# Kernel tuning notes

Hardware: AMD Instinct MI355X
Metric: run time of the kernel (lower is better)

## Reference

```python
import jax, jax.numpy as jnp
import numpy as np

MEM, KD, VD, H, TEMP = 4096, 512, 512, 8, 1.0
B, N, BW = 4, 1024, 1024


def setup_inputs() -> dict:
    key = jax.random.key(0)
    ks = jax.random.split(key, 9)
    s = 0.02
    return {
        "queries": jax.random.normal(ks[0], (B, N, KD), jnp.float32),
        "write_keys": jax.random.normal(ks[1], (BW, KD), jnp.float32),
        "write_values": jax.random.normal(ks[2], (BW, VD), jnp.float32),
        "mem_keys": jax.random.normal(ks[3], (MEM, KD), jnp.float32),
        "mem_values": jax.random.normal(ks[4], (MEM, VD), jnp.float32),
        "Wq": jax.random.normal(ks[5], (KD, KD * H), jnp.float32) * s,
        "bq": jnp.zeros((KD * H,), jnp.float32),
        "Wvp": jax.random.normal(ks[6], (H * VD, VD), jnp.float32) * s,
        "bvp": jnp.zeros((VD,), jnp.float32),
        "Wg": jax.random.normal(ks[7], (KD + VD, KD), jnp.float32) * s,
        "bg": jnp.zeros((KD,), jnp.float32),
    }


def _read(queries, mem_keys, mem_values, Wq, bq, Wvp, bvp):
    b, n, _ = queries.shape
    q = queries @ Wq + bq                       # [b, n, H*KD]
    q = q.reshape(b, n, H, KD).transpose(0, 2, 1, 3)  # [b, h, n, d]
    # keys/values are shared across batch & heads: contract directly, no repeat
    scores = jnp.einsum('bhnd,md->bhnm', q, mem_keys) / (KD ** 0.5) / TEMP
    attn = jax.nn.softmax(scores, axis=-1)
    rv = jnp.einsum('bhnm,md->bhnd', attn, mem_values)  # [b, h, n, VD]
    rv = rv.transpose(0, 2, 1, 3).reshape(b, n, H * VD)
    return rv @ Wvp + bvp                        # [b, n, VD]


def _write(write_keys, write_values, mem_keys, mem_values, Wg, bg):
    eps = 1e-8
    kn = write_keys / jnp.maximum(jnp.linalg.norm(write_keys, axis=-1, keepdims=True), eps)
    mn = mem_keys / jnp.maximum(jnp.linalg.norm(mem_keys, axis=-1, keepdims=True), eps)
    idx = jnp.argmax(kn @ mn.T, axis=1)          # [BW] fixed against original keys

    def step(carry, inp):
        K, V = carry
        k, v, i = inp
        combined = jnp.concatenate([k, V[i]], axis=-1)   # reads current values
        gate = jax.nn.sigmoid(combined @ Wg + bg)        # [KD]
        K = K.at[i].set(gate * k + (1.0 - gate) * K[i])
        V = V.at[i].set(gate * v + (1.0 - gate) * V[i])
        return (K, V), None

    (nk, nv), _ = jax.lax.scan(step, (mem_keys, mem_values), (write_keys, write_values, idx))
    return nk, nv


def reference(queries, write_keys, write_values, mem_keys, mem_values, Wq, bq, Wvp, bvp, Wg, bg):
    read_out = _read(queries, mem_keys, mem_values, Wq, bq, Wvp, bvp)
    new_keys, new_values = _write(write_keys, write_values, mem_keys, mem_values, Wg, bg)
    return read_out, new_keys, new_values
```

## Files before the change

kernel.cpp:

```cpp
#include <hip/hip_runtime.h>
#include <cstdint>
#include <cstddef>

typedef __attribute__((ext_vector_type(8))) short short8;
typedef __attribute__((ext_vector_type(4))) float f32x4;
typedef __attribute__((ext_vector_type(4))) int i32x4;
typedef __attribute__((ext_vector_type(8))) int i32x8;
typedef unsigned char u8;
typedef unsigned short u16;
typedef unsigned int u32;
typedef unsigned long long u64;

__device__ __forceinline__ u16 f2bf(float f) {
    u32 u = __float_as_uint(f);
    u = (u + 0x7FFFu + ((u >> 16) & 1u)) >> 16;
    return (u16)u;
}
__device__ __forceinline__ float bf2f(u16 h) {
    u32 u = ((u32)h) << 16;
    return __uint_as_float(u);
}
__device__ __forceinline__ u8 f2fp8(float f) {
    return (u8)(__builtin_amdgcn_cvt_pk_fp8_f32(f, f, 0, false) & 0xFF);
}

__device__ __forceinline__ void gl_lds16(const void* g, void* l) {
    __builtin_amdgcn_global_load_lds((const __attribute__((address_space(1))) void*)g,
                                     (__attribute__((address_space(3))) void*)l, 16, 0, 0);
}

__global__ void cast_bf16_kernel(const float* __restrict__ src, u16* __restrict__ dst) {
    int i = blockIdx.x * 256 + threadIdx.x;
    float4 v = *((const float4*)src + i);
    ushort4 r;
    r.x = f2bf(v.x); r.y = f2bf(v.y); r.z = f2bf(v.z); r.w = f2bf(v.w);
    *((ushort4*)dst + i) = r;
}

__global__ void split_bf16_kernel(const float* __restrict__ src,
                                  u16* __restrict__ hi, u16* __restrict__ lo) {
    int i = blockIdx.x * 256 + threadIdx.x;
    float4 v = *((const float4*)src + i);
    ushort4 h, l;
    h.x = f2bf(v.x); l.x = f2bf(v.x - bf2f(h.x));
    h.y = f2bf(v.y); l.y = f2bf(v.y - bf2f(h.y));
    h.z = f2bf(v.z); l.z = f2bf(v.z - bf2f(h.z));
    h.w = f2bf(v.w); l.w = f2bf(v.w - bf2f(h.w));
    *((ushort4*)hi + i) = h;
    *((ushort4*)lo + i) = l;
}

__global__ void cast_transpose_kernel(const float* __restrict__ src, u16* __restrict__ dst,
                                      int R, int C) {
    __shared__ float tile[32][33];
    int tx = threadIdx.x & 31, ty = threadIdx.x >> 5;
    int c0 = blockIdx.x * 32, r0 = blockIdx.y * 32;
#pragma unroll
    for (int j = 0; j < 4; j++)
        tile[ty + 8 * j][tx] = src[(size_t)(r0 + ty + 8 * j) * C + c0 + tx];
    __syncthreads();
#pragma unroll
    for (int j = 0; j < 4; j++)
        dst[(size_t)(c0 + ty + 8 * j) * R + r0 + tx] = f2bf(tile[tx][ty + 8 * j]);
}

__global__ void cast_transpose_fp8_kernel(const float* __restrict__ src, u8* __restrict__ dst,
                                          int R, int C) {
    __shared__ float tile[32][33];
    int tx = threadIdx.x & 31, ty = threadIdx.x >> 5;
    int c0 = blockIdx.x * 32, r0 = blockIdx.y * 32;
#pragma unroll
    for (int j = 0; j < 4; j++)
        tile[ty + 8 * j][tx] = src[(size_t)(r0 + ty + 8 * j) * C + c0 + tx];
    __syncthreads();
#pragma unroll
    for (int j = 0; j < 4; j++)
        dst[(size_t)(c0 + ty + 8 * j) * R + r0 + tx] = f2fp8(tile[tx][ty + 8 * j]);
}

__global__ __launch_bounds__(256) void key_prep_kernel(const float* __restrict__ mk,
                                                       u16* __restrict__ mn_hi,
                                                       u16* __restrict__ mn_lo,
                                                       u16* __restrict__ Kb) {
    int row = blockIdx.x, tid = threadIdx.x;
    const float* src = mk + (size_t)row * 512;
    float x0 = src[tid], x1 = src[tid + 256];
    float ss = x0 * x0 + x1 * x1;
#pragma unroll
    for (int m = 1; m < 64; m <<= 1) ss += __shfl_xor(ss, m);
    __shared__ float sred[4];
    if ((tid & 63) == 0) sred[tid >> 6] = ss;
    __syncthreads();
    float tot = sred[0] + sred[1] + sred[2] + sred[3];
    float inv = 1.0f / fmaxf(sqrtf(tot), 1e-8f);
    float n0 = x0 * inv, n1 = x1 * inv;
    u16 h0 = f2bf(n0), h1 = f2bf(n1);
    mn_hi[(size_t)row * 512 + tid] = h0;
    mn_hi[(size_t)row * 512 + tid + 256] = h1;
    mn_lo[(size_t)row * 512 + tid] = f2bf(n0 - bf2f(h0));
    mn_lo[(size_t)row * 512 + tid + 256] = f2bf(n1 - bf2f(h1));
    Kb[(size_t)row * 512 + tid] = f2bf(x0);
    Kb[(size_t)row * 512 + tid + 256] = f2bf(x1);
}

template <int BN, int EPI>
__global__ __launch_bounds__(256, 2) void gemm_bt_kernel(const u16* __restrict__ A,
                                                         const u16* __restrict__ Bt,
                                                         const float* __restrict__ bias,
                                                         void* __restrict__ Cout,
                                                         int M, int N, int K) {
    constexpr int NT = BN / 32;
    __shared__ __align__(16) u16 A_lds[128 * 32];
    __shared__ __align__(16) u16 B_lds[BN * 32];
    int tid = threadIdx.x;
    int w = tid >> 6, lane = tid & 63, l15 = lane & 15, quad = lane >> 4;
    int wm = w >> 1, wn = w & 1;
    int n0 = blockIdx.x * BN, m0 = blockIdx.y * 128;
    int sa = (l15 >> 1) & 3;

    f32x4 acc[4][NT];
#pragma unroll
    for (int i = 0; i < 4; i++)
#pragma unroll
        for (int j = 0; j < NT; j++) acc[i][j] = (f32x4)(0.0f);

    for (int kt = 0; kt < K; kt += 32) {
        __syncthreads();
#pragma unroll
        for (int i = 0; i < 2; i++) {
            int c = i * 256 + tid;
            int r = c >> 2, s = (c & 3) ^ ((r >> 1) & 3);
            gl_lds16(&A[(size_t)(m0 + r) * K + kt + s * 8], &A_lds[c * 8]);
        }
#pragma unroll
        for (int i = 0; i < BN / 64; i++) {
            int c = i * 256 + tid;
            int r = c >> 2, s = (c & 3) ^ ((r >> 1) & 3);
            gl_lds16(&Bt[(size_t)(n0 + r) * K + kt + s * 8], &B_lds[c * 8]);
        }
        __syncthreads();
        short8 af[4], bf[NT];
#pragma unroll
        for (int mt = 0; mt < 4; mt++)
            af[mt] = *(const short8*)&A_lds[(wm * 64 + mt * 16 + l15) * 32 + (quad ^ sa) * 8];
#pragma unroll
        for (int nt = 0; nt < NT; nt++)
            bf[nt] = *(const short8*)&B_lds[(wn * (BN / 2) + nt * 16 + l15) * 32 + (quad ^ sa) * 8];
#pragma unroll
        for (int mt = 0; mt < 4; mt++)
#pragma unroll
            for (int nt = 0; nt < NT; nt++)
                acc[mt][nt] = __builtin_amdgcn_mfma_f32_16x16x32_bf16(af[mt], bf[nt], acc[mt][nt], 0, 0, 0);
    }

#pragma unroll
    for (int nt = 0; nt < NT; nt++) {
        int col = n0 + wn * (BN / 2) + nt * 16 + l15;
        float bs = bias[col];
#pragma unroll
        for (int mt = 0; mt < 4; mt++) {
            int row = m0 + wm * 64 + mt * 16 + quad * 4;
#pragma unroll
            for (int r = 0; r < 4; r++) {
                float v = acc[mt][nt][r] + bs;
                if (EPI == 0) {
                    ((float*)Cout)[(size_t)(row + r) * N + col] = v;
                } else {
                    int rr = row + r;
                    int bi = rr >> 10, ni = rr & 1023;
                    int h = col >> 9, d = col & 511;
                    ((u16*)Cout)[(((size_t)((bi * 8 + h)) * 1024 + ni)) * 512 + d] = f2bf(v);
                }
            }
        }
    }
}

__global__ __launch_bounds__(256, 2) void s_exp_gemm_kernel(const u16* __restrict__ Q,
                                                            const u16* __restrict__ Kb,
                                                            u8* __restrict__ P,
                                                            float* __restrict__ denom) {
    __shared__ __align__(16) u16 A_lds[128 * 32];
    __shared__ __align__(16) u16 B_lds[128 * 32];
    int tid = threadIdx.x;
    int w = tid >> 6, lane = tid & 63, l15 = lane & 15, quad = lane >> 4;
    int wm = w >> 1, wn = w & 1;
    int s0 = blockIdx.x * 128, q0 = blockIdx.y * 128;
    int sa = (l15 >> 1) & 3;

    f32x4 acc[4][4];
#pragma unroll
    for (int i = 0; i < 4; i++)
#pragma unroll
        for (int j = 0; j < 4; j++) acc[i][j] = (f32x4)(0.0f);

    for (int kt = 0; kt < 512; kt += 32) {
        __syncthreads();
#pragma unroll
        for (int i = 0; i < 2; i++) {
            int c = i * 256 + tid;
            int r = c >> 2, s = (c & 3) ^ ((r >> 1) & 3);
            gl_lds16(&Kb[(size_t)(s0 + r) * 512 + kt + s * 8], &A_lds[c * 8]);
            gl_lds16(&Q[(size_t)(q0 + r) * 512 + kt + s * 8], &B_lds[c * 8]);
        }
        __syncthreads();
        short8 af[4], bf[4];
#pragma unroll
        for (int mt = 0; mt < 4; mt++)
            af[mt] = *(const short8*)&A_lds[(wm * 64 + mt * 16 + l15) * 32 + (quad ^ sa) * 8];
#pragma unroll
        for (int nt = 0; nt < 4; nt++)
            bf[nt] = *(const short8*)&B_lds[(wn * 64 + nt * 16 + l15) * 32 + (quad ^ sa) * 8];
#pragma unroll
        for (int mt = 0; mt < 4; mt++)
#pragma unroll
            for (int nt = 0; nt < 4; nt++)
                acc[mt][nt] = __builtin_amdgcn_mfma_f32_16x16x32_bf16(af[mt], bf[nt], acc[mt][nt], 0, 0, 0);
    }

    const float sc = 0.06375871826463886f;
#pragma unroll
    for (int nt = 0; nt < 4; nt++) {
        int q = q0 + wn * 64 + nt * 16 + l15;
        float rs = 0.f;
#pragma unroll
        for (int mt = 0; mt < 4; mt++) {
            float p0 = exp2f(acc[mt][nt][0] * sc);
            float p1 = exp2f(acc[mt][nt][1] * sc);
            float p2 = exp2f(acc[mt][nt][2] * sc);
            float p3 = exp2f(acc[mt][nt][3] * sc);
            rs += (p0 + p1) + (p2 + p3);
            u32 lo = (u32)__builtin_amdgcn_cvt_pk_fp8_f32(p0, p1, 0, false);
            u32 dw = (u32)__builtin_amdgcn_cvt_pk_fp8_f32(p2, p3, (int)lo, true);
            int col = s0 + wm * 64 + mt * 16 + quad * 4;
            *(u32*)&P[(size_t)q * 4096 + col] = dw;
        }
        rs += __shfl_xor(rs, 16);
        rs += __shfl_xor(rs, 32);
        if (quad == 0) atomicAdd(&denom[q], rs);
    }
}

__global__ __launch_bounds__(256, 2) void pv_gemm_kernel(const u8* __restrict__ P,
                                                         const u8* __restrict__ Vt8,
                                                         const float* __restrict__ denom,
                                                         u16* __restrict__ rv,
                                                         int bh0) {
    __shared__ __align__(16) u8 A_lds[128 * 128];
    __shared__ __align__(16) u8 B_lds[128 * 128];
    int tid = threadIdx.x;
    int w = tid >> 6, lane = tid & 63, l15 = lane & 15, quad = lane >> 4;
    int wm = w >> 1, wn = w & 1;
    int d0 = blockIdx.x * 128, q0 = blockIdx.y * 128;

    f32x4 acc[4][4];
#pragma unroll
    for (int i = 0; i < 4; i++)
#pragma unroll
        for (int j = 0; j < 4; j++) acc[i][j] = (f32x4)(0.0f);

    for (int kt = 0; kt < 4096; kt += 128) {
        __syncthreads();
#pragma unroll
        for (int i = 0; i < 4; i++) {
            int c = i * 256 + tid;
            int r = c >> 3, s = (c & 7) ^ (r & 7);
            gl_lds16(&Vt8[(size_t)(d0 + r) * 4096 + kt + s * 16], &A_lds[c * 16]);
            gl_lds16(&P[(size_t)(q0 + r) * 4096 + kt + s * 16], &B_lds[c * 16]);
        }
        __syncthreads();
        i32x8 af[4], bf[4];
#pragma unroll
        for (int mt = 0; mt < 4; mt++) {
            int row = wm * 64 + mt * 16 + l15;
            const u8* pa = &A_lds[row * 128];
            int sl0 = (quad * 2) ^ (row & 7), sl1 = (quad * 2 + 1) ^ (row & 7);
            i32x4 lo = *(const i32x4*)&pa[sl0 * 16];
            i32x4 hi = *(const i32x4*)&pa[sl1 * 16];
            af[mt] = __builtin_shufflevector(lo, hi, 0, 1, 2, 3, 4, 5, 6, 7);
        }
#pragma unroll
        for (int nt = 0; nt < 4; nt++) {
            int row = wn * 64 + nt * 16 + l15;
            const u8* pb = &B_lds[row * 128];
            int sl0 = (quad * 2) ^ (row & 7), sl1 = (quad * 2 + 1) ^ (row & 7);
            i32x4 lo = *(const i32x4*)&pb[sl0 * 16];
            i32x4 hi = *(const i32x4*)&pb[sl1 * 16];
            bf[nt] = __builtin_shufflevector(lo, hi, 0, 1, 2, 3, 4, 5, 6, 7);
        }
#pragma unroll
        for (int mt = 0; mt < 4; mt++)
#pragma unroll
            for (int nt = 0; nt < 4; nt++)
                acc[mt][nt] = __builtin_amdgcn_mfma_scale_f32_16x16x128_f8f6f4(
                    af[mt], bf[nt], acc[mt][nt], 0, 0,
                    0, 0x7F7F7F7F, 0, 0x7F7F7F7F);
    }

#pragma unroll
    for (int nt = 0; nt < 4; nt++) {
        int lq = q0 + wn * 64 + nt * 16 + l15;
        int gr = bh0 * 1024 + lq;
        float inv = 1.0f / denom[lq];
        int b = gr >> 13, h = (gr >> 10) & 7, n = gr & 1023;
        size_t base = ((size_t)(b * 1024 + n)) * 4096 + h * 512;
#pragma unroll
        for (int mt = 0; mt < 4; mt++) {
            int d = d0 + wm * 64 + mt * 16 + quad * 4;
            ushort4 v4;
            v4.x = f2bf(acc[mt][nt][0] * inv);
            v4.y = f2bf(acc[mt][nt][1] * inv);
            v4.z = f2bf(acc[mt][nt][2] * inv);
            v4.w = f2bf(acc[mt][nt][3] * inv);
            *(ushort4*)&rv[base + d] = v4;
        }
    }
}

__global__ __launch_bounds__(256, 2) void sims_mfma_kernel(const u16* __restrict__ Ah,
                                                           const u16* __restrict__ Al,
                                                           const u16* __restrict__ Bh,
                                                           const u16* __restrict__ Bl,
                                                           u64* __restrict__ amax) {
    __shared__ __align__(16) u16 Ah_lds[128 * 32];
    __shared__ __align__(16) u16 Al_lds[128 * 32];
    __shared__ __align__(16) u16 Bh_lds[128 * 32];
    __shared__ __align__(16) u16 Bl_lds[128 * 32];
    int tid = threadIdx.x;
    int w = tid >> 6, lane = tid & 63, l15 = lane & 15, quad = lane >> 4;
    int wm = w >> 1, wn = w & 1;
    int n0 = blockIdx.x * 128, m0 = blockIdx.y * 128;
    int sa = (l15 >> 1) & 3;

    f32x4 acc[4][4];
#pragma unroll
    for (int i = 0; i < 4; i++)
#pragma unroll
        for (int j = 0; j < 4; j++) acc[i][j] = (f32x4)(0.0f);

    for (int kt = 0; kt < 512; kt += 32) {
        __syncthreads();
#pragma unroll
        for (int i = 0; i < 2; i++) {
            int c = i * 256 + tid;
            int r = c >> 2, s = (c & 3) ^ ((r >> 1) & 3);
            size_t ga = (size_t)(m0 + r) * 512 + kt + s * 8;
            size_t gb = (size_t)(n0 + r) * 512 + kt + s * 8;
            gl_lds16(&Ah[ga], &Ah_lds[c * 8]);
            gl_lds16(&Al[ga], &Al_lds[c * 8]);
            gl_lds16(&Bh[gb], &Bh_lds[c * 8]);
            gl_lds16(&Bl[gb], &Bl_lds[c * 8]);
        }
        __syncthreads();
        short8 afh[4], afl[4], bfh[4], bfl[4];
#pragma unroll
        for (int mt = 0; mt < 4; mt++) {
            int off = (wm * 64 + mt * 16 + l15) * 32 + (quad ^ sa) * 8;
            afh[mt] = *(const short8*)&Ah_lds[off];
            afl[mt] = *(const short8*)&Al_lds[off];
        }
#pragma unroll
        for (int nt = 0; nt < 4; nt++) {
            int off = (wn * 64 + nt * 16 + l15) * 32 + (quad ^ sa) * 8;
            bfh[nt] = *(const short8*)&Bh_lds[off];
            bfl[nt] = *(const short8*)&Bl_lds[off];
        }
#pragma unroll
        for (int mt = 0; mt < 4; mt++)
#pragma unroll
            for (int nt = 0; nt < 4; nt++) {
                acc[mt][nt] = __builtin_amdgcn_mfma_f32_16x16x32_bf16(afh[mt], bfh[nt], acc[mt][nt], 0, 0, 0);
                acc[mt][nt] = __builtin_amdgcn_mfma_f32_16x16x32_bf16(afh[mt], bfl[nt], acc[mt][nt], 0, 0, 0);
                acc[mt][nt] = __builtin_amdgcn_mfma_f32_16x16x32_bf16(afl[mt], bfh[nt], acc[mt][nt], 0, 0, 0);
            }
    }

#pragma unroll
    for (int mt = 0; mt < 4; mt++) {
#pragma unroll
        for (int r = 0; r < 4; r++) {
            int row = m0 + wm * 64 + mt * 16 + quad * 4 + r;
            u64 best = 0;
#pragma unroll
            for (int nt = 0; nt < 4; nt++) {
                int col = n0 + wn * 64 + nt * 16 + l15;
                u32 bb = __float_as_uint(acc[mt][nt][r]);
                bb = (bb & 0x80000000u) ? ~bb : (bb | 0x80000000u);
                u64 key = ((u64)bb << 32) | (u32)(4095 - col);
                best = best > key ? best : key;
            }
            u64 o;
            o = __shfl_xor(best, 1); best = best > o ? best : o;
            o = __shfl_xor(best, 2); best = best > o ? best : o;
            o = __shfl_xor(best, 4); best = best > o ? best : o;
            o = __shfl_xor(best, 8); best = best > o ? best : o;
            if (l15 == 0) atomicMax(&amax[row], best);
        }
    }
}

__global__ __launch_bounds__(64) void chains_build_kernel(const u64* __restrict__ amax,
                                                          int* __restrict__ idx,
                                                          int* __restrict__ nxt,
                                                          int* __restrict__ heads,
                                                          int* __restrict__ count) {
    __shared__ int sidx[1024];
    int tid = threadIdx.x;
    for (int j = tid; j < 1024; j += 64)
        sidx[j] = 4095 - (int)(u32)(amax[j] & 0xFFFFFFFFull);
    __syncthreads();
    int i = blockIdx.x * 64 + tid;
    int my = sidx[i];
    idx[i] = my;
    int nx = -1;
    for (int j = i + 1; j < 1024; j++)
        if (sidx[j] == my) { nx = j; break; }
    nxt[i] = nx;
    bool head = true;
    for (int j = 0; j < i; j++)
        if (sidx[j] == my) { head = false; break; }
    if (head) {
        int p = atomicAdd(count, 1);
        heads[p] = i;
    }
}

__global__ __launch_bounds__(256) void g1_gemm_kernel(const float* __restrict__ wk,
                                                      const float* __restrict__ Wg,
                                                      const float* __restrict__ bg,
                                                      float* __restrict__ G1) {
    __shared__ float wkl[8][512];
    int tid = threadIdx.x;
    int i0 = blockIdx.x * 8;
    for (int i = tid; i < 8 * 512; i += 256) wkl[i >> 9][i & 511] = wk[(size_t)i0 * 512 + i];
    __syncthreads();
    float a0[8], a1[8];
#pragma unroll
    for (int i = 0; i < 8; i++) { a0[i] = 0.f; a1[i] = 0.f; }
    for (int c = 0; c < 512; c++) {
        float w0 = Wg[(size_t)c * 512 + tid];
        float w1 = Wg[(size_t)c * 512 + tid + 256];
#pragma unroll
        for (int ii = 0; ii < 8; ii++) {
            float s = wkl[ii][c];
            a0[ii] += s * w0; a1[ii] += s * w1;
        }
    }
    float b0 = bg[tid], b1 = bg[tid + 256];
#pragma unroll
    for (int ii = 0; ii < 8; ii++) {
        G1[(size_t)(i0 + ii) * 512 + tid] = a0[ii] + b0;
        G1[(size_t)(i0 + ii) * 512 + tid + 256] = a1[ii] + b1;
    }
}

__global__ __launch_bounds__(256) void chain_apply_kernel(const int* __restrict__ heads,
                                                          const int* __restrict__ count,
                                                          const int* __restrict__ idx,
                                                          const int* __restrict__ nxt,
                                                          const float* __restrict__ G1,
                                                          const float* __restrict__ Wg,
                                                          const float* __restrict__ wk,
                                                          const float* __restrict__ wv,
                                                          const float* __restrict__ mk,
                                                          const float* __restrict__ mv,
                                                          float* __restrict__ outK,
                                                          float* __restrict__ outV) {
    int b = blockIdx.x;
    if (b >= *count) return;
    int i = heads[b];
    int s = idx[i];
    int tid = threadIdx.x;
    __shared__ float V[512];
    V[tid] = mv[(size_t)s * 512 + tid];
    V[tid + 256] = mv[(size_t)s * 512 + tid + 256];
    float k0 = mk[(size_t)s * 512 + tid], k1 = mk[(size_t)s * 512 + tid + 256];
    __syncthreads();
    while (i >= 0) {
        float a0 = G1[(size_t)i * 512 + tid], a1 = G1[(size_t)i * 512 + tid + 256];
        for (int c = 0; c < 512; c++) {
            float vc = V[c];
            a0 += vc * Wg[(size_t)(512 + c) * 512 + tid];
            a1 += vc * Wg[(size_t)(512 + c) * 512 + tid + 256];
        }
        float g0 = 1.f / (1.f + __expf(-a0));
        float g1 = 1.f / (1.f + __expf(-a1));
        __syncthreads();
        k0 = g0 * wk[(size_t)i * 512 + tid] + (1.f - g0) * k0;
        k1 = g1 * wk[(size_t)i * 512 + tid + 256] + (1.f - g1) * k1;
        V[tid] = g0 * wv[(size_t)i * 512 + tid] + (1.f - g0) * V[tid];
        V[tid + 256] = g1 * wv[(size_t)i * 512 + tid + 256] + (1.f - g1) * V[tid + 256];
        __syncthreads();
        i = nxt[i];
    }
    outK[(size_t)s * 512 + tid] = k0;
    outK[(size_t)s * 512 + tid + 256] = k1;
    outV[(size_t)s * 512 + tid] = V[tid];
    outV[(size_t)s * 512 + tid + 256] = V[tid + 256];
}

extern "C" void kernel_launch(void* const* d_in, const int* in_sizes, int n_in,
                              void* d_out, int out_size, void* d_ws, size_t ws_size,
                              hipStream_t stream) {
    const float* queries = (const float*)d_in[0];
    const float* wkeys   = (const float*)d_in[1];
    const float* wvals   = (const float*)d_in[2];
    const float* mkeys   = (const float*)d_in[3];
    const float* mvals   = (const float*)d_in[4];
    const float* Wq      = (const float*)d_in[5];
    const float* bq      = (const float*)d_in[6];
    const float* Wvp     = (const float*)d_in[7];
    const float* bvp     = (const float*)d_in[8];
    const float* Wg      = (const float*)d_in[9];
    const float* bg      = (const float*)d_in[10];

    float* out_read = (float*)d_out;
    float* out_k = out_read + (size_t)4 * 1024 * 512;
    float* out_v = out_k + (size_t)4096 * 512;

    char* ws = (char*)d_ws;
    const size_t MB = 1024 * 1024;
    u16* Qbf  = (u16*)(ws);
    u16* WqT  = (u16*)(ws + 4 * MB);
    u16* Qatt = (u16*)(ws + 8 * MB);
    u16* Kb   = (u16*)(ws + 40 * MB);
    u8*  Vt8  = (u8*)(ws + 44 * MB);
    u16* rv   = (u16*)(ws + 48 * MB);
    u16* WvpT = (u16*)(ws + 80 * MB);
    u16* mn_hi = (u16*)(ws + 84 * MB);
    u16* mn_lo = (u16*)(ws + 88 * MB);
    float* G1  = (float*)(ws + 92 * MB);
    u16* wk_hi = (u16*)(ws + 94 * MB);
    u16* wk_lo = (u16*)(ws + 95 * MB);
    u64* amax   = (u64*)(ws);
    int* count  = (int*)(ws + 8192);
    int* idx    = (int*)(ws + 8192 + 256);
    int* nxt    = (int*)(ws + 8192 + 256 + 4096);
    int* heads  = (int*)(ws + 8192 + 256 + 8192);
    float* denom = (float*)(ws + 32 * 1024);
    u8* P = (u8*)(ws + 84 * MB);
    (void)in_sizes; (void)n_in; (void)out_size;

    size_t avail = (ws_size > 84 * MB) ? ws_size - 84 * MB : 0;
    int G = 2;
    for (int g = 32; g >= 2; g >>= 1)
        if ((size_t)g * 4 * MB <= avail) { G = g; break; }

    hipMemcpyAsync(out_k, mkeys, (size_t)4096 * 512 * 4, hipMemcpyDeviceToDevice, stream);
    hipMemcpyAsync(out_v, mvals, (size_t)4096 * 512 * 4, hipMemcpyDeviceToDevice, stream);

    cast_bf16_kernel<<<2048, 256, 0, stream>>>(queries, Qbf);
    cast_transpose_kernel<<<dim3(4096 / 32, 512 / 32), 256, 0, stream>>>(Wq, WqT, 512, 4096);
    cast_transpose_kernel<<<dim3(512 / 32, 4096 / 32), 256, 0, stream>>>(Wvp, WvpT, 4096, 512);
    cast_transpose_fp8_kernel<<<dim3(512 / 32, 4096 / 32), 256, 0, stream>>>(mvals, Vt8, 4096, 512);
    key_prep_kernel<<<4096, 256, 0, stream>>>(mkeys, mn_hi, mn_lo, Kb);
    split_bf16_kernel<<<512, 256, 0, stream>>>(wkeys, wk_hi, wk_lo);

    gemm_bt_kernel<128, 1><<<dim3(32, 32), 256, 0, stream>>>(Qbf, WqT, bq, (void*)Qatt, 4096, 4096, 512);

    hipMemsetAsync(ws, 0, 8192 + 256, stream);
    hipMemsetAsync(denom, 0, 32768 * 4, stream);
    sims_mfma_kernel<<<dim3(32, 8), 256, 0, stream>>>(wk_hi, wk_lo, mn_hi, mn_lo, amax);
    chains_build_kernel<<<16, 64, 0, stream>>>(amax, idx, nxt, heads, count);
    g1_gemm_kernel<<<128, 256, 0, stream>>>(wkeys, Wg, bg, G1);
    chain_apply_kernel<<<1024, 256, 0, stream>>>(heads, count, idx, nxt, G1, Wg,
                                                 wkeys, wvals, mkeys, mvals, out_k, out_v);

    for (int bh0 = 0; bh0 < 32; bh0 += G) {
        const u16* Achunk = Qatt + (size_t)bh0 * 1024 * 512;
        float* dchunk = denom + bh0 * 1024;
        s_exp_gemm_kernel<<<dim3(32, G * 8), 256, 0, stream>>>(Achunk, Kb, P, dchunk);
        pv_gemm_kernel<<<dim3(4, G * 8), 256, 0, stream>>>(P, Vt8, dchunk, rv, bh0);
    }

    gemm_bt_kernel<64, 0><<<dim3(8, 32), 256, 0, stream>>>(rv, WvpT, bvp, (void*)out_read, 4096, 512, 4096);
}
```

Measured before the change: 752.8 us.

## Double-buffer LDS tiles in the GEMM, score and PV kernels

Converts the three MFMA GEMM kernels (projection GEMM, score/exp GEMM, fp8 PV GEMM) from single-buffered LDS tiles with two barriers per k-step to double-buffered tiles with one barrier per step. The next tile's global-to-LDS loads are issued before the current tile's MFMAs, so load latency can overlap compute. Per-thread source pointers and LDS offsets are hoisted out of the loop. The cost is twice the LDS per block (64KB in the PV kernel), which may limit occupancy, and it relies on the barrier also waiting for outstanding async LDS loads.

```diff
diff --git a/kernel.cpp b/kernel.cpp
--- a/kernel.cpp
+++ b/kernel.cpp
@@ -110,42 +110,58 @@
                                                          void* __restrict__ Cout,
                                                          int M, int N, int K) {
     constexpr int NT = BN / 32;
-    __shared__ __align__(16) u16 A_lds[128 * 32];
-    __shared__ __align__(16) u16 B_lds[BN * 32];
+    __shared__ __align__(16) u16 A_lds[2][128 * 32];
+    __shared__ __align__(16) u16 B_lds[2][BN * 32];
     int tid = threadIdx.x;
     int w = tid >> 6, lane = tid & 63, l15 = lane & 15, quad = lane >> 4;
     int wm = w >> 1, wn = w & 1;
     int n0 = blockIdx.x * BN, m0 = blockIdx.y * 128;
     int sa = (l15 >> 1) & 3;
 
+    const u16* srcA[2]; int ldsA[2];
+    const u16* srcB[BN / 64]; int ldsB[BN / 64];
+#pragma unroll
+    for (int i = 0; i < 2; i++) {
+        int c = i * 256 + tid, r = c >> 2, s = (c & 3) ^ ((r >> 1) & 3);
+        srcA[i] = &A[(size_t)(m0 + r) * K + s * 8];
+        ldsA[i] = c * 8;
+    }
+#pragma unroll
+    for (int i = 0; i < BN / 64; i++) {
+        int c = i * 256 + tid, r = c >> 2, s = (c & 3) ^ ((r >> 1) & 3);
+        srcB[i] = &Bt[(size_t)(n0 + r) * K + s * 8];
+        ldsB[i] = c * 8;
+    }
+
     f32x4 acc[4][NT];
 #pragma unroll
     for (int i = 0; i < 4; i++)
 #pragma unroll
         for (int j = 0; j < NT; j++) acc[i][j] = (f32x4)(0.0f);
 
-    for (int kt = 0; kt < K; kt += 32) {
+    int nk = K >> 5;
+#pragma unroll
+    for (int i = 0; i < 2; i++) gl_lds16(srcA[i], &A_lds[0][ldsA[i]]);
+#pragma unroll
+    for (int i = 0; i < BN / 64; i++) gl_lds16(srcB[i], &B_lds[0][ldsB[i]]);
+
+    for (int t = 0; t < nk; t++) {
         __syncthreads();
-#pragma unroll
-        for (int i = 0; i < 2; i++) {
-            int c = i * 256 + tid;
-            int r = c >> 2, s = (c & 3) ^ ((r >> 1) & 3);
-            gl_lds16(&A[(size_t)(m0 + r) * K + kt + s * 8], &A_lds[c * 8]);
-        }
-#pragma unroll
-        for (int i = 0; i < BN / 64; i++) {
-            int c = i * 256 + tid;
-            int r = c >> 2, s = (c & 3) ^ ((r >> 1) & 3);
-            gl_lds16(&Bt[(size_t)(n0 + r) * K + kt + s * 8], &B_lds[c * 8]);
-        }
-        __syncthreads();
+        int cur = t & 1;
+        if (t + 1 < nk) {
+            int koff = (t + 1) * 32;
+#pragma unroll
+            for (int i = 0; i < 2; i++) gl_lds16(srcA[i] + koff, &A_lds[cur ^ 1][ldsA[i]]);
+#pragma unroll
+            for (int i = 0; i < BN / 64; i++) gl_lds16(srcB[i] + koff, &B_lds[cur ^ 1][ldsB[i]]);
+        }
         short8 af[4], bf[NT];
 #pragma unroll
         for (int mt = 0; mt < 4; mt++)
-            af[mt] = *(const short8*)&A_lds[(wm * 64 + mt * 16 + l15) * 32 + (quad ^ sa) * 8];
+            af[mt] = *(const short8*)&A_lds[cur][(wm * 64 + mt * 16 + l15) * 32 + (quad ^ sa) * 8];
 #pragma unroll
         for (int nt = 0; nt < NT; nt++)
-            bf[nt] = *(const short8*)&B_lds[(wn * (BN / 2) + nt * 16 + l15) * 32 + (quad ^ sa) * 8];
+            bf[nt] = *(const short8*)&B_lds[cur][(wn * (BN / 2) + nt * 16 + l15) * 32 + (quad ^ sa) * 8];
 #pragma unroll
         for (int mt = 0; mt < 4; mt++)
 #pragma unroll
@@ -180,37 +196,53 @@
                                                             const u16* __restrict__ Kb,
                                                             u8* __restrict__ P,
                                                             float* __restrict__ denom) {
-    __shared__ __align__(16) u16 A_lds[128 * 32];
-    __shared__ __align__(16) u16 B_lds[128 * 32];
+    __shared__ __align__(16) u16 A_lds[2][128 * 32];
+    __shared__ __align__(16) u16 B_lds[2][128 * 32];
     int tid = threadIdx.x;
     int w = tid >> 6, lane = tid & 63, l15 = lane & 15, quad = lane >> 4;
     int wm = w >> 1, wn = w & 1;
     int s0 = blockIdx.x * 128, q0 = blockIdx.y * 128;
     int sa = (l15 >> 1) & 3;
 
+    const u16* srcA[2]; const u16* srcB[2]; int ldsO[2];
+#pragma unroll
+    for (int i = 0; i < 2; i++) {
+        int c = i * 256 + tid, r = c >> 2, s = (c & 3) ^ ((r >> 1) & 3);
+        srcA[i] = &Kb[(size_t)(s0 + r) * 512 + s * 8];
+        srcB[i] = &Q[(size_t)(q0 + r) * 512 + s * 8];
+        ldsO[i] = c * 8;
+    }
+
     f32x4 acc[4][4];
 #pragma unroll
     for (int i = 0; i < 4; i++)
 #pragma unroll
         for (int j = 0; j < 4; j++) acc[i][j] = (f32x4)(0.0f);
 
-    for (int kt = 0; kt < 512; kt += 32) {
+#pragma unroll
+    for (int i = 0; i < 2; i++) {
+        gl_lds16(srcA[i], &A_lds[0][ldsO[i]]);
+        gl_lds16(srcB[i], &B_lds[0][ldsO[i]]);
+    }
+
+    for (int t = 0; t < 16; t++) {
         __syncthreads();
-#pragma unroll
-        for (int i = 0; i < 2; i++) {
-            int c = i * 256 + tid;
-            int r = c >> 2, s = (c & 3) ^ ((r >> 1) & 3);
-            gl_lds16(&Kb[(size_t)(s0 + r) * 512 + kt + s * 8], &A_lds[c * 8]);
-            gl_lds16(&Q[(size_t)(q0 + r) * 512 + kt + s * 8], &B_lds[c * 8]);
-        }
-        __syncthreads();
+        int cur = t & 1;
+        if (t < 15) {
+            int koff = (t + 1) * 32;
+#pragma unroll
+            for (int i = 0; i < 2; i++) {
+                gl_lds16(srcA[i] + koff, &A_lds[cur ^ 1][ldsO[i]]);
+                gl_lds16(srcB[i] + koff, &B_lds[cur ^ 1][ldsO[i]]);
+            }
+        }
         short8 af[4], bf[4];
 #pragma unroll
         for (int mt = 0; mt < 4; mt++)
-            af[mt] = *(const short8*)&A_lds[(wm * 64 + mt * 16 + l15) * 32 + (quad ^ sa) * 8];
+            af[mt] = *(const short8*)&A_lds[cur][(wm * 64 + mt * 16 + l15) * 32 + (quad ^ sa) * 8];
 #pragma unroll
         for (int nt = 0; nt < 4; nt++)
-            bf[nt] = *(const short8*)&B_lds[(wn * 64 + nt * 16 + l15) * 32 + (quad ^ sa) * 8];
+            bf[nt] = *(const short8*)&B_lds[cur][(wn * 64 + nt * 16 + l15) * 32 + (quad ^ sa) * 8];
 #pragma unroll
         for (int mt = 0; mt < 4; mt++)
 #pragma unroll
@@ -246,34 +278,50 @@
                                                          const float* __restrict__ denom,
                                                          u16* __restrict__ rv,
                                                          int bh0) {
-    __shared__ __align__(16) u8 A_lds[128 * 128];
-    __shared__ __align__(16) u8 B_lds[128 * 128];
+    __shared__ __align__(16) u8 A_lds[2][128 * 128];
+    __shared__ __align__(16) u8 B_lds[2][128 * 128];
     int tid = threadIdx.x;
     int w = tid >> 6, lane = tid & 63, l15 = lane & 15, quad = lane >> 4;
     int wm = w >> 1, wn = w & 1;
     int d0 = blockIdx.x * 128, q0 = blockIdx.y * 128;
 
+    const u8* srcA[4]; const u8* srcB[4]; int ldsO[4];
+#pragma unroll
+    for (int i = 0; i < 4; i++) {
+        int c = i * 256 + tid, r = c >> 3, s = (c & 7) ^ (r & 7);
+        srcA[i] = &Vt8[(size_t)(d0 + r) * 4096 + s * 16];
+        srcB[i] = &P[(size_t)(q0 + r) * 4096 + s * 16];
+        ldsO[i] = c * 16;
+    }
+
     f32x4 acc[4][4];
 #pragma unroll
     for (int i = 0; i < 4; i++)
 #pragma unroll
         for (int j = 0; j < 4; j++) acc[i][j] = (f32x4)(0.0f);
 
-    for (int kt = 0; kt < 4096; kt += 128) {
+#pragma unroll
+    for (int i = 0; i < 4; i++) {
+        gl_lds16(srcA[i], &A_lds[0][ldsO[i]]);
+        gl_lds16(srcB[i], &B_lds[0][ldsO[i]]);
+    }
+
+    for (int t = 0; t < 32; t++) {
         __syncthreads();
-#pragma unroll
-        for (int i = 0; i < 4; i++) {
-            int c = i * 256 + tid;
-            int r = c >> 3, s = (c & 7) ^ (r & 7);
-            gl_lds16(&Vt8[(size_t)(d0 + r) * 4096 + kt + s * 16], &A_lds[c * 16]);
-            gl_lds16(&P[(size_t)(q0 + r) * 4096 + kt + s * 16], &B_lds[c * 16]);
-        }
-        __syncthreads();
+        int cur = t & 1;
+        if (t < 31) {
+            int koff = (t + 1) * 128;
+#pragma unroll
+            for (int i = 0; i < 4; i++) {
+                gl_lds16(srcA[i] + koff, &A_lds[cur ^ 1][ldsO[i]]);
+                gl_lds16(srcB[i] + koff, &B_lds[cur ^ 1][ldsO[i]]);
+            }
+        }
         i32x8 af[4], bf[4];
 #pragma unroll
         for (int mt = 0; mt < 4; mt++) {
             int row = wm * 64 + mt * 16 + l15;
-            const u8* pa = &A_lds[row * 128];
+            const u8* pa = &A_lds[cur][row * 128];
             int sl0 = (quad * 2) ^ (row & 7), sl1 = (quad * 2 + 1) ^ (row & 7);
             i32x4 lo = *(const i32x4*)&pa[sl0 * 16];
             i32x4 hi = *(const i32x4*)&pa[sl1 * 16];
@@ -282,7 +330,7 @@
 #pragma unroll
         for (int nt = 0; nt < 4; nt++) {
             int row = wn * 64 + nt * 16 + l15;
-            const u8* pb = &B_lds[row * 128];
+            const u8* pb = &B_lds[cur][row * 128];
             int sl0 = (quad * 2) ^ (row & 7), sl1 = (quad * 2 + 1) ^ (row & 7);
             i32x4 lo = *(const i32x4*)&pb[sl0 * 16];
             i32x4 hi = *(const i32x4*)&pb[sl1 * 16];
```

Measured after the change: 785.4 us. +4.3%, slower.

## Split-K the output projection GEMM and widen the score GEMM's K tile

Applied to the files above, without the earlier changes.

The final rv @ Wvp projection (M=4096, N=512, K=4096) now runs as a split-K kernel with four K slices, accumulating into a zeroed output with float atomics. This raises the grid from 256 to 1024 blocks so more of the GPU is busy. Separately, the score/exp GEMM now loads 64-wide K tiles with an 8-way XOR swizzle, halving the number of barrier pairs per tile. The costs are an extra memset, atomic traffic and nondeterministic summation order, plus doubled LDS use in the score kernel.

```diff
diff --git a/kernel.cpp b/kernel.cpp
--- a/kernel.cpp
+++ b/kernel.cpp
@@ -176,17 +176,78 @@
     }
 }
 
+__global__ __launch_bounds__(256, 2) void gemm_bt_splitk_kernel(const u16* __restrict__ A,
+                                                                const u16* __restrict__ Bt,
+                                                                const float* __restrict__ bias,
+                                                                float* __restrict__ C,
+                                                                int M, int N, int K, int Kc) {
+    __shared__ __align__(16) u16 A_lds[128 * 32];
+    __shared__ __align__(16) u16 B_lds[64 * 32];
+    int tid = threadIdx.x;
+    int w = tid >> 6, lane = tid & 63, l15 = lane & 15, quad = lane >> 4;
+    int wm = w >> 1, wn = w & 1;
+    int n0 = blockIdx.x * 64, m0 = blockIdx.y * 128;
+    int k0 = blockIdx.z * Kc;
+    int sa = (l15 >> 1) & 3;
+
+    f32x4 acc[4][2];
+#pragma unroll
+    for (int i = 0; i < 4; i++)
+#pragma unroll
+        for (int j = 0; j < 2; j++) acc[i][j] = (f32x4)(0.0f);
+
+    for (int kt = k0; kt < k0 + Kc; kt += 32) {
+        __syncthreads();
+#pragma unroll
+        for (int i = 0; i < 2; i++) {
+            int c = i * 256 + tid;
+            int r = c >> 2, s = (c & 3) ^ ((r >> 1) & 3);
+            gl_lds16(&A[(size_t)(m0 + r) * K + kt + s * 8], &A_lds[c * 8]);
+        }
+        {
+            int c = tid;
+            int r = c >> 2, s = (c & 3) ^ ((r >> 1) & 3);
+            gl_lds16(&Bt[(size_t)(n0 + r) * K + kt + s * 8], &B_lds[c * 8]);
+        }
+        __syncthreads();
+        short8 af[4], bf[2];
+#pragma unroll
+        for (int mt = 0; mt < 4; mt++)
+            af[mt] = *(const short8*)&A_lds[(wm * 64 + mt * 16 + l15) * 32 + (quad ^ sa) * 8];
+#pragma unroll
+        for (int nt = 0; nt < 2; nt++)
+            bf[nt] = *(const short8*)&B_lds[(wn * 32 + nt * 16 + l15) * 32 + (quad ^ sa) * 8];
+#pragma unroll
+        for (int mt = 0; mt < 4; mt++)
+#pragma unroll
+            for (int nt = 0; nt < 2; nt++)
+                acc[mt][nt] = __builtin_amdgcn_mfma_f32_16x16x32_bf16(af[mt], bf[nt], acc[mt][nt], 0, 0, 0);
+    }
+
+#pragma unroll
+    for (int nt = 0; nt < 2; nt++) {
+        int col = n0 + wn * 32 + nt * 16 + l15;
+        float bs = (blockIdx.z == 0) ? bias[col] : 0.0f;
+#pragma unroll
+        for (int mt = 0; mt < 4; mt++) {
+            int row = m0 + wm * 64 + mt * 16 + quad * 4;
+#pragma unroll
+            for (int r = 0; r < 4; r++)
+                atomicAdd(&C[(size_t)(row + r) * N + col], acc[mt][nt][r] + bs);
+        }
+    }
+}
+
 __global__ __launch_bounds__(256, 2) void s_exp_gemm_kernel(const u16* __restrict__ Q,
                                                             const u16* __restrict__ Kb,
                                                             u8* __restrict__ P,
                                                             float* __restrict__ denom) {
-    __shared__ __align__(16) u16 A_lds[128 * 32];
-    __shared__ __align__(16) u16 B_lds[128 * 32];
+    __shared__ __align__(16) u16 A_lds[128 * 64];
+    __shared__ __align__(16) u16 B_lds[128 * 64];
     int tid = threadIdx.x;
     int w = tid >> 6, lane = tid & 63, l15 = lane & 15, quad = lane >> 4;
     int wm = w >> 1, wn = w & 1;
     int s0 = blockIdx.x * 128, q0 = blockIdx.y * 128;
-    int sa = (l15 >> 1) & 3;
 
     f32x4 acc[4][4];
 #pragma unroll
@@ -194,28 +255,35 @@
 #pragma unroll
         for (int j = 0; j < 4; j++) acc[i][j] = (f32x4)(0.0f);
 
-    for (int kt = 0; kt < 512; kt += 32) {
-        __syncthreads();
-#pragma unroll
-        for (int i = 0; i < 2; i++) {
+    for (int kt = 0; kt < 512; kt += 64) {
+        __syncthreads();
+#pragma unroll
+        for (int i = 0; i < 4; i++) {
             int c = i * 256 + tid;
-            int r = c >> 2, s = (c & 3) ^ ((r >> 1) & 3);
+            int r = c >> 3, s = (c & 7) ^ (r & 7);
             gl_lds16(&Kb[(size_t)(s0 + r) * 512 + kt + s * 8], &A_lds[c * 8]);
             gl_lds16(&Q[(size_t)(q0 + r) * 512 + kt + s * 8], &B_lds[c * 8]);
         }
         __syncthreads();
-        short8 af[4], bf[4];
-#pragma unroll
-        for (int mt = 0; mt < 4; mt++)
-            af[mt] = *(const short8*)&A_lds[(wm * 64 + mt * 16 + l15) * 32 + (quad ^ sa) * 8];
-#pragma unroll
-        for (int nt = 0; nt < 4; nt++)
-            bf[nt] = *(const short8*)&B_lds[(wn * 64 + nt * 16 + l15) * 32 + (quad ^ sa) * 8];
-#pragma unroll
-        for (int mt = 0; mt < 4; mt++)
-#pragma unroll
-            for (int nt = 0; nt < 4; nt++)
-                acc[mt][nt] = __builtin_amdgcn_mfma_f32_16x16x32_bf16(af[mt], bf[nt], acc[mt][nt], 0, 0, 0);
+#pragma unroll
+        for (int kk = 0; kk < 2; kk++) {
+            short8 af[4], bf[4];
+#pragma unroll
+            for (int mt = 0; mt < 4; mt++) {
+                int row = wm * 64 + mt * 16 + l15;
+                af[mt] = *(const short8*)&A_lds[row * 64 + (((kk * 4 + quad) ^ (row & 7)) * 8)];
+            }
+#pragma unroll
+            for (int nt = 0; nt < 4; nt++) {
+                int row = wn * 64 + nt * 16 + l15;
+                bf[nt] = *(const short8*)&B_lds[row * 64 + (((kk * 4 + quad) ^ (row & 7)) * 8)];
+            }
+#pragma unroll
+            for (int mt = 0; mt < 4; mt++)
+#pragma unroll
+                for (int nt = 0; nt < 4; nt++)
+                    acc[mt][nt] = __builtin_amdgcn_mfma_f32_16x16x32_bf16(af[mt], bf[nt], acc[mt][nt], 0, 0, 0);
+        }
     }
 
     const float sc = 0.06375871826463886f;
@@ -548,6 +616,7 @@
 
     hipMemcpyAsync(out_k, mkeys, (size_t)4096 * 512 * 4, hipMemcpyDeviceToDevice, stream);
     hipMemcpyAsync(out_v, mvals, (size_t)4096 * 512 * 4, hipMemcpyDeviceToDevice, stream);
+    hipMemsetAsync(out_read, 0, (size_t)4 * 1024 * 512 * 4, stream);
 
     cast_bf16_kernel<<<2048, 256, 0, stream>>>(queries, Qbf);
     cast_transpose_kernel<<<dim3(4096 / 32, 512 / 32), 256, 0, stream>>>(Wq, WqT, 512, 4096);
@@ -573,5 +642,6 @@
         pv_gemm_kernel<<<dim3(4, G * 8), 256, 0, stream>>>(P, Vt8, dchunk, rv, bh0);
     }
 
-    gemm_bt_kernel<64, 0><<<dim3(8, 32), 256, 0, stream>>>(rv, WvpT, bvp, (void*)out_read, 4096, 512, 4096);
-}
+    gemm_bt_splitk_kernel<<<dim3(8, 32, 4), 256, 0, stream>>>(rv, WvpT, bvp, out_read,
+                                                              4096, 512, 4096, 1024);
+}
```

After: 759.8 us. No clear change (+0.9%).
